# Kernel tuning notes

Hardware: AMD Instinct MI355X
Metric: run time of the kernel (lower is better)

Reference implementation:

```python
import jax, jax.numpy as jnp
import numpy as np

D = 1024
H = 16
HD = D // H
B = 4
L = 2048
FFN = 4 * D
EPS = 1e-5


def _layer_norm(x, g, b):
    mu = jnp.mean(x, axis=-1, keepdims=True)
    var = jnp.mean(jnp.square(x - mu), axis=-1, keepdims=True)
    return (x - mu) * jax.lax.rsqrt(var + EPS) * g + b


def setup_inputs() -> dict:
    key = jax.random.key(0)
    ks = jax.random.split(key, 16)
    s = 1.0 / np.sqrt(D)
    inp = {
        "x": jax.random.normal(ks[0], (B, L, D), dtype=jnp.float32),
        "rel_pos_bias": jax.random.normal(ks[1], (1, H, L, L), dtype=jnp.float32) * 0.02,
        "wq": jax.random.normal(ks[2], (D, D), dtype=jnp.float32) * s,
        "bq": jnp.zeros((D,), jnp.float32),
        "wk": jax.random.normal(ks[3], (D, D), dtype=jnp.float32) * s,
        "bk": jnp.zeros((D,), jnp.float32),
        "wv": jax.random.normal(ks[4], (D, D), dtype=jnp.float32) * s,
        "bv": jnp.zeros((D,), jnp.float32),
        "wo": jax.random.normal(ks[5], (D, D), dtype=jnp.float32) * s,
        "bo": jnp.zeros((D,), jnp.float32),
        "g1": jnp.ones((D,), jnp.float32),
        "be1": jnp.zeros((D,), jnp.float32),
        "g2": jnp.ones((D,), jnp.float32),
        "be2": jnp.zeros((D,), jnp.float32),
        "w1": jax.random.normal(ks[6], (D, FFN), dtype=jnp.float32) * s,
        "bf1": jnp.zeros((FFN,), jnp.float32),
        "w2": jax.random.normal(ks[7], (FFN, D), dtype=jnp.float32) * (1.0 / np.sqrt(FFN)),
        "bf2": jnp.zeros((D,), jnp.float32),
    }
    return inp


def reference(x, rel_pos_bias, wq, bq, wk, bk, wv, bv, wo, bo,
              g1, be1, g2, be2, w1, bf1, w2, bf2):
    scale = HD ** -0.5
    residual = x
    xn = _layer_norm(x, g1, be1)
    # projections -> (B, H, L, HD)
    q = (xn @ wq + bq).reshape(B, L, H, HD).transpose(0, 2, 1, 3)
    k = (xn @ wk + bk).reshape(B, L, H, HD).transpose(0, 2, 1, 3)
    v = (xn @ wv + bv).reshape(B, L, H, HD).transpose(0, 2, 1, 3)
    scores = jnp.einsum('bhqd,bhkd->bhqk', q, k) * scale
    causal = jnp.tril(jnp.ones((L, L), dtype=bool))
    scores = jnp.where(causal[None, None], scores, -jnp.inf)
    scores = scores + rel_pos_bias
    attn = jax.nn.softmax(scores, axis=-1)
    out = jnp.einsum('bhqk,bhkd->bhqd', attn, v)
    out = out.transpose(0, 2, 1, 3).reshape(B, L, D)
    out = out @ wo + bo
    x = residual + out
    residual = x
    xn = _layer_norm(x, g2, be2)
    h = jax.nn.relu(xn @ w1 + bf1)
    x = residual + (h @ w2 + bf2)
    return x
```

## Files before the change

### kernel.cpp

```cpp
#include <hip/hip_runtime.h>
#include <hip/hip_bf16.h>

#define D_   1024
#define H_   16
#define HD_  64
#define B_   4
#define L_   2048
#define FFN_ 4096
#define M_   (B_ * L_)

typedef __bf16 bf16x8 __attribute__((ext_vector_type(8)));
typedef float f32x4 __attribute__((ext_vector_type(4)));
typedef unsigned short ushort8 __attribute__((ext_vector_type(8)));
typedef unsigned short ushort4v __attribute__((ext_vector_type(4)));

__device__ inline unsigned short f2bf(float f) {
    unsigned int u = __float_as_uint(f);
    u += 0x7fff + ((u >> 16) & 1);
    return (unsigned short)(u >> 16);
}
__device__ inline float bf2f(unsigned short u) {
    return __uint_as_float(((unsigned int)u) << 16);
}

__device__ inline void gl_lds16(const unsigned short* g, unsigned short* l) {
    __builtin_amdgcn_global_load_lds(
        (const __attribute__((address_space(1))) unsigned int*)g,
        (__attribute__((address_space(3))) unsigned int*)l, 16, 0, 0);
}

__global__ __launch_bounds__(256) void k_transpose_bf16(
    const float* __restrict__ in, unsigned short* __restrict__ out, int K, int N)
{
    __shared__ float tile[64][65];
    int k0 = blockIdx.y * 64, n0 = blockIdx.x * 64;
    int t = threadIdx.x;
    int r = t >> 2, cs = (t & 3) * 16;
    const float* src = in + (size_t)(k0 + r) * N + n0 + cs;
#pragma unroll
    for (int i = 0; i < 16; i += 4) {
        float4 v = *(const float4*)(src + i);
        tile[r][cs + i + 0] = v.x;
        tile[r][cs + i + 1] = v.y;
        tile[r][cs + i + 2] = v.z;
        tile[r][cs + i + 3] = v.w;
    }
    __syncthreads();
    unsigned short* dst = out + (size_t)(n0 + r) * K + k0 + cs;
#pragma unroll
    for (int i = 0; i < 16; ++i) dst[i] = f2bf(tile[cs + i][r]);
}

__global__ void k_concat_bias(const float* __restrict__ bq, const float* __restrict__ bk,
                              const float* __restrict__ bv, float* __restrict__ out)
{
    int i = blockIdx.x * 256 + threadIdx.x;
    float v = (i < 1024) ? bq[i] : (i < 2048 ? bk[i - 1024] : bv[i - 2048]);
    out[i] = v;
}

__global__ __launch_bounds__(256) void k_layernorm(
    const float* __restrict__ x, const float* __restrict__ g, const float* __restrict__ be,
    unsigned short* __restrict__ out)
{
    int row = blockIdx.x;
    const float* xr = x + (size_t)row * D_;
    int t = threadIdx.x;
    float4 v = *(const float4*)(xr + t * 4);
    float s = v.x + v.y + v.z + v.w;
    float sq = v.x * v.x + v.y * v.y + v.z * v.z + v.w * v.w;
#pragma unroll
    for (int off = 32; off >= 1; off >>= 1) {
        s  += __shfl_down(s, off);
        sq += __shfl_down(sq, off);
    }
    __shared__ float ps[4], psq[4];
    int w = t >> 6;
    if ((t & 63) == 0) { ps[w] = s; psq[w] = sq; }
    __syncthreads();
    float tot  = ps[0] + ps[1] + ps[2] + ps[3];
    float totq = psq[0] + psq[1] + psq[2] + psq[3];
    float mu  = tot * (1.f / D_);
    float var = totq * (1.f / D_) - mu * mu;
    float inv = rsqrtf(var + 1e-5f);
    float4 gv = *(const float4*)(g + t * 4);
    float4 bv = *(const float4*)(be + t * 4);
    ushort4v o;
    o[0] = f2bf((v.x - mu) * inv * gv.x + bv.x);
    o[1] = f2bf((v.y - mu) * inv * gv.y + bv.y);
    o[2] = f2bf((v.z - mu) * inv * gv.z + bv.z);
    o[3] = f2bf((v.w - mu) * inv * gv.w + bv.w);
    *(ushort4v*)(out + (size_t)row * D_ + t * 4) = o;
}

template <int BN, int WGN, bool OUT_BF16, bool RELU, bool RESID>
__global__ __launch_bounds__(512, 2) void k_gemm2(
    const unsigned short* __restrict__ A, const unsigned short* __restrict__ Bt,
    const float* __restrict__ bias, const float* __restrict__ resid,
    void* __restrict__ Cout, int M, int N, int K)
{
    constexpr int WGM = 8 / WGN;
    constexpr int MS = 256 / WGM;
    constexpr int NS = BN / WGN;
    constexpr int MI = MS / 16;
    constexpr int NI = NS / 16;

    __shared__ unsigned short sA[2][256 * 32];
    __shared__ unsigned short sB[2][BN * 32];

    int nwg = gridDim.x, flat = blockIdx.x;
    int wg = (flat & 7) * (nwg >> 3) + (flat >> 3);
    int gx = N / BN;
    int m0 = (wg / gx) * 256, n0 = (wg % gx) * BN;

    int tid = threadIdx.x, lane = tid & 63, wv = tid >> 6;
    int wr = wv / WGN, wc = wv % WGN;
    int wm = wr * MS, wn = wc * NS;
    int lr = lane & 15, qd = lane >> 4;

    f32x4 acc[MI][NI] = {};

    int srow = lane >> 2, scol = (lane & 3) * 8;
    const unsigned short* gA0 = A + (size_t)(m0 + wv * 16 + srow) * K + scol;
    const unsigned short* gA1 = gA0 + (size_t)128 * K;
    const unsigned short* gB0 = Bt + (size_t)(n0 + wv * 16 + srow) * K + scol;
    const unsigned short* gB1 = gB0 + (size_t)128 * K;
    int lb0 = (wv * 16) * 32, lb1 = (wv * 16 + 128) * 32;

    gl_lds16(gA0, &sA[0][lb0]);
    gl_lds16(gA1, &sA[0][lb1]);
    gl_lds16(gB0, &sB[0][lb0]);
    if constexpr (BN == 256) gl_lds16(gB1, &sB[0][lb1]);

    int nk = K >> 5;
    for (int ki = 0; ki < nk; ++ki) {
        int cur = ki & 1;
        __syncthreads();
        if (ki + 1 < nk) {
            int k1 = (ki + 1) << 5;
            gl_lds16(gA0 + k1, &sA[cur ^ 1][lb0]);
            gl_lds16(gA1 + k1, &sA[cur ^ 1][lb1]);
            gl_lds16(gB0 + k1, &sB[cur ^ 1][lb0]);
            if constexpr (BN == 256) gl_lds16(gB1 + k1, &sB[cur ^ 1][lb1]);
        }
        bf16x8 af[MI], bfr[NI];
#pragma unroll
        for (int i = 0; i < MI; ++i)
            af[i] = *(const bf16x8*)(&sA[cur][(wm + i * 16 + lr) * 32 + qd * 8]);
#pragma unroll
        for (int i = 0; i < NI; ++i)
            bfr[i] = *(const bf16x8*)(&sB[cur][(wn + i * 16 + lr) * 32 + qd * 8]);
        __builtin_amdgcn_s_setprio(1);
#pragma unroll
        for (int mi = 0; mi < MI; ++mi)
#pragma unroll
            for (int ni = 0; ni < NI; ++ni)
                acc[mi][ni] = __builtin_amdgcn_mfma_f32_16x16x32_bf16(
                    af[mi], bfr[ni], acc[mi][ni], 0, 0, 0);
        __builtin_amdgcn_s_setprio(0);
    }

#pragma unroll
    for (int ni = 0; ni < NI; ++ni) {
        int col = n0 + wn + ni * 16 + lr;
        float bvv = bias[col];
#pragma unroll
        for (int mi = 0; mi < MI; ++mi) {
#pragma unroll
            for (int r = 0; r < 4; ++r) {
                int row = m0 + wm + mi * 16 + qd * 4 + r;
                float v = acc[mi][ni][r] + bvv;
                if (RELU) v = fmaxf(v, 0.f);
                if (RESID) v += resid[(size_t)row * N + col];
                if (OUT_BF16)
                    ((unsigned short*)Cout)[(size_t)row * N + col] = f2bf(v);
                else
                    ((float*)Cout)[(size_t)row * N + col] = v;
            }
        }
    }
}

__global__ __launch_bounds__(256, 4) void k_attn(
    const unsigned short* __restrict__ qkv, const float* __restrict__ rpb,
    unsigned short* __restrict__ out)
{
    __shared__ unsigned short Ks[64 * 72];
    __shared__ unsigned short Vt[64 * 64];
    __shared__ unsigned short Sp[64 * 72];

    int flat = blockIdx.x;
    int xcd = flat & 7, b = (flat >> 3) & 3, hi = flat >> 5;
    int g = hi * 8 + xcd;
    int h = g & 15;
    int qt = 31 - (g >> 4);
    int q0 = qt * 64;

    int t = threadIdx.x, lane = t & 63, w = t >> 6;
    int lr = lane & 15, qd = lane >> 4;
    int sr = t >> 2, ss = (t & 3) * 16;
    int bL = b * L_;

    bf16x8 aq[2];
    {
        const unsigned short* qsrc =
            qkv + (size_t)(bL + q0 + w * 16 + lr) * 3072 + h * 64 + qd * 8;
        aq[0] = *(const bf16x8*)qsrc;
        aq[1] = *(const bf16x8*)(qsrc + 32);
    }

    f32x4 oacc[4] = {};
    float m_r[4], l_r[4];
#pragma unroll
    for (int r = 0; r < 4; ++r) { m_r[r] = -1e30f; l_r[r] = 0.f; }

    int qrow_base = q0 + w * 16 + qd * 4;
    int ntile = qt + 1;

    ushort8 krA, krB, vrA, vrB;
    {
        const unsigned short* kb_ = qkv + (size_t)(bL + sr) * 3072 + 1024 + h * 64 + ss;
        krA = *(const ushort8*)kb_;  krB = *(const ushort8*)(kb_ + 8);
        vrA = *(const ushort8*)(kb_ + 1024); vrB = *(const ushort8*)(kb_ + 1032);
    }

    for (int kt = 0; kt < ntile; ++kt) {
        int k0 = kt * 64;
        if (kt) __syncthreads();

        *(ushort8*)(Ks + sr * 72 + ss)     = krA;
        *(ushort8*)(Ks + sr * 72 + ss + 8) = krB;

        {
            int role = sr & 1;
            int srp  = sr & ~1;
#pragma unroll
            for (int i = 0; i < 8; ++i) {
                int sendv = role ? (int)(unsigned int)vrA[i] : (int)(unsigned int)vrB[i];
                int got = __shfl_xor(sendv, 4);
                int d = role ? (ss + 8 + i) : (ss + i);
                unsigned short lo = role ? (unsigned short)got : vrA[i];
                unsigned short hi = role ? vrB[i] : (unsigned short)got;
                int swz = (d ^ (d >> 3)) & 7;
                unsigned int u = (unsigned int)lo | ((unsigned int)hi << 16);
                *(unsigned int*)(Vt + d * 64 + (srp ^ (swz << 3))) = u;
            }
        }
        __syncthreads();

        float rv[4][4];
        {
            const float* rpb_base = rpb + ((size_t)h * L_ + qrow_base) * L_ + k0;
#pragma unroll
            for (int r = 0; r < 4; ++r)
#pragma unroll
                for (int nt = 0; nt < 4; ++nt)
                    rv[r][nt] = rpb_base[(size_t)r * L_ + nt * 16 + lr];
        }

        if (kt + 1 < ntile) {
            const unsigned short* kb_ =
                qkv + (size_t)(bL + k0 + 64 + sr) * 3072 + 1024 + h * 64 + ss;
            krA = *(const ushort8*)kb_;  krB = *(const ushort8*)(kb_ + 8);
            vrA = *(const ushort8*)(kb_ + 1024); vrB = *(const ushort8*)(kb_ + 1032);
        }

        f32x4 sc4[4] = {};
        __builtin_amdgcn_s_setprio(1);
#pragma unroll
        for (int ks = 0; ks < 2; ++ks) {
#pragma unroll
            for (int nt = 0; nt < 4; ++nt) {
                bf16x8 bk8 = *(const bf16x8*)(Ks + (nt * 16 + lr) * 72 + ks * 32 + qd * 8);
                sc4[nt] = __builtin_amdgcn_mfma_f32_16x16x32_bf16(aq[ks], bk8, sc4[nt], 0, 0, 0);
            }
        }
        __builtin_amdgcn_s_setprio(0);

        bool last = (kt == qt);
        float pvv[4][4], mx[4];
#pragma unroll
        for (int r = 0; r < 4; ++r) {
            mx[r] = -1e30f;
#pragma unroll
            for (int nt = 0; nt < 4; ++nt) {
                float sv = sc4[nt][r] * 0.125f + rv[r][nt];
                if (last && (k0 + nt * 16 + lr > qrow_base + r)) sv = -1e30f;
                pvv[r][nt] = sv;
                mx[r] = fmaxf(mx[r], sv);
            }
        }
#pragma unroll
        for (int r = 0; r < 4; ++r) {
            mx[r] = fmaxf(mx[r], __shfl_xor(mx[r], 1));
            mx[r] = fmaxf(mx[r], __shfl_xor(mx[r], 2));
            mx[r] = fmaxf(mx[r], __shfl_xor(mx[r], 4));
            mx[r] = fmaxf(mx[r], __shfl_xor(mx[r], 8));
        }
#pragma unroll
        for (int r = 0; r < 4; ++r) {
            float mnew  = fmaxf(m_r[r], mx[r]);
            float alpha = __expf(m_r[r] - mnew);
            float psum = 0.f;
#pragma unroll
            for (int nt = 0; nt < 4; ++nt) {
                float p = __expf(pvv[r][nt] - mnew);
                psum += p;
                Sp[(w * 16 + qd * 4 + r) * 72 + nt * 16 + lr] = f2bf(p);
            }
            psum += __shfl_xor(psum, 1);
            psum += __shfl_xor(psum, 2);
            psum += __shfl_xor(psum, 4);
            psum += __shfl_xor(psum, 8);
            l_r[r] = l_r[r] * alpha + psum;
            m_r[r] = mnew;
            oacc[0][r] *= alpha; oacc[1][r] *= alpha;
            oacc[2][r] *= alpha; oacc[3][r] *= alpha;
        }

        __builtin_amdgcn_s_setprio(1);
#pragma unroll
        for (int ks = 0; ks < 2; ++ks) {
            bf16x8 ap = *(const bf16x8*)(Sp + (w * 16 + lr) * 72 + ks * 32 + qd * 8);
#pragma unroll
            for (int dt = 0; dt < 4; ++dt) {
                int d = dt * 16 + lr;
                int swz = (d ^ (d >> 3)) & 7;
                bf16x8 bv8 = *(const bf16x8*)(Vt + d * 64 + ((ks * 32 + qd * 8) ^ (swz << 3)));
                oacc[dt] = __builtin_amdgcn_mfma_f32_16x16x32_bf16(ap, bv8, oacc[dt], 0, 0, 0);
            }
        }
        __builtin_amdgcn_s_setprio(0);
    }

#pragma unroll
    for (int r = 0; r < 4; ++r) {
        float linv = 1.f / l_r[r];
        int qrow = q0 + w * 16 + qd * 4 + r;
        unsigned short* dst = out + (size_t)(bL + qrow) * 1024 + h * 64;
#pragma unroll
        for (int dt = 0; dt < 4; ++dt)
            dst[dt * 16 + lr] = f2bf(oacc[dt][r] * linv);
    }
}

extern "C" void kernel_launch(void* const* d_in, const int* in_sizes, int n_in,
                              void* d_out, int out_size, void* d_ws, size_t ws_size,
                              hipStream_t stream)
{
    const float* x   = (const float*)d_in[0];
    const float* rpb = (const float*)d_in[1];
    const float* wq  = (const float*)d_in[2];
    const float* bq  = (const float*)d_in[3];
    const float* wk  = (const float*)d_in[4];
    const float* bk  = (const float*)d_in[5];
    const float* wv  = (const float*)d_in[6];
    const float* bv  = (const float*)d_in[7];
    const float* wo  = (const float*)d_in[8];
    const float* bo  = (const float*)d_in[9];
    const float* g1  = (const float*)d_in[10];
    const float* be1 = (const float*)d_in[11];
    const float* g2  = (const float*)d_in[12];
    const float* be2 = (const float*)d_in[13];
    const float* w1  = (const float*)d_in[14];
    const float* bf1 = (const float*)d_in[15];
    const float* w2  = (const float*)d_in[16];
    const float* bf2 = (const float*)d_in[17];
    float* out = (float*)d_out;
    char* ws = (char*)d_ws;

    unsigned short* xn1   = (unsigned short*)(ws + 0);
    unsigned short* qkv   = (unsigned short*)(ws + 16777216);
    unsigned short* attno = (unsigned short*)(ws + 0);
    unsigned short* hbuf  = (unsigned short*)(ws + 0);
    float*          xmid  = (float*)(ws + 67108864);
    unsigned short* xn2   = (unsigned short*)(ws + 100663296);
    unsigned short* wqkvT = (unsigned short*)(ws + 117440512);
    unsigned short* woT   = (unsigned short*)(ws + 123731968);
    unsigned short* w1T   = (unsigned short*)(ws + 125829120);
    unsigned short* w2T   = (unsigned short*)(ws + 134217728);
    float*          bqkv  = (float*)(ws + 142606336);

    k_transpose_bf16<<<dim3(16, 16), 256, 0, stream>>>(wq, wqkvT,                1024, 1024);
    k_transpose_bf16<<<dim3(16, 16), 256, 0, stream>>>(wk, wqkvT + 1024 * 1024,  1024, 1024);
    k_transpose_bf16<<<dim3(16, 16), 256, 0, stream>>>(wv, wqkvT + 2048 * 1024,  1024, 1024);
    k_transpose_bf16<<<dim3(16, 16), 256, 0, stream>>>(wo, woT,                  1024, 1024);
    k_transpose_bf16<<<dim3(64, 16), 256, 0, stream>>>(w1, w1T,                  1024, 4096);
    k_transpose_bf16<<<dim3(16, 64), 256, 0, stream>>>(w2, w2T,                  4096, 1024);
    k_concat_bias<<<12, 256, 0, stream>>>(bq, bk, bv, bqkv);

    k_layernorm<<<M_, 256, 0, stream>>>(x, g1, be1, xn1);
    k_gemm2<128, 2, true, false, false><<<dim3(768), 512, 0, stream>>>(
        xn1, wqkvT, bqkv, nullptr, qkv, M_, 3072, 1024);
    k_attn<<<dim3(2048), 256, 0, stream>>>(qkv, rpb, attno);
    k_gemm2<128, 2, false, false, true><<<dim3(256), 512, 0, stream>>>(
        attno, woT, bo, x, xmid, M_, 1024, 1024);
    k_layernorm<<<M_, 256, 0, stream>>>(xmid, g2, be2, xn2);
    k_gemm2<256, 4, true, true, false><<<dim3(512), 512, 0, stream>>>(
        xn2, w1T, bf1, nullptr, hbuf, M_, 4096, 1024);
    k_gemm2<128, 2, false, false, true><<<dim3(256), 512, 0, stream>>>(
        hbuf, w2T, bf2, xmid, out, M_, 1024, 4096);
}
```

Baseline: 896.1 us.

## Rewrite GEMM with K=64 stages, XOR-swizzled LDS, and templated tile shapes

Replaces the GEMM kernel with a generalized template that stages 64-wide K slices instead of 32, writes LDS with an XOR swizzle to avoid bank conflicts on fragment reads, and parameterizes block and wave tile shapes. The QKV GEMM moves to 256x256 tiles, and the N=1024 GEMMs move to 128x128 tiles with 256 threads and more blocks. Halving the number of K iterations cuts barrier overhead, and the swizzle targets LDS read conflicts. The cost is doubled LDS per buffer and different occupancy per shape.

```diff
diff --git a/kernel.cpp b/kernel.cpp
--- a/kernel.cpp
+++ b/kernel.cpp
@@ -18,9 +18,6 @@
     unsigned int u = __float_as_uint(f);
     u += 0x7fff + ((u >> 16) & 1);
     return (unsigned short)(u >> 16);
-}
-__device__ inline float bf2f(unsigned short u) {
-    return __uint_as_float(((unsigned int)u) << 16);
 }
 
 __device__ inline void gl_lds16(const unsigned short* g, unsigned short* l) {
@@ -93,71 +90,93 @@
     *(ushort4v*)(out + (size_t)row * D_ + t * 4) = o;
 }
 
-template <int BN, int WGN, bool OUT_BF16, bool RELU, bool RESID>
-__global__ __launch_bounds__(512, 2) void k_gemm2(
+template <int BM, int BN, int WM, int WN, bool OUT_BF16, bool RELU, bool RESID>
+__global__ __launch_bounds__(WM * WN * 64, 2) void k_gemm3(
     const unsigned short* __restrict__ A, const unsigned short* __restrict__ Bt,
     const float* __restrict__ bias, const float* __restrict__ resid,
     void* __restrict__ Cout, int M, int N, int K)
 {
-    constexpr int WGM = 8 / WGN;
-    constexpr int MS = 256 / WGM;
-    constexpr int NS = BN / WGN;
-    constexpr int MI = MS / 16;
-    constexpr int NI = NS / 16;
-
-    __shared__ unsigned short sA[2][256 * 32];
-    __shared__ unsigned short sB[2][BN * 32];
+    constexpr int NW  = WM * WN;
+    constexpr int MS  = BM / WM;
+    constexpr int NS  = BN / WN;
+    constexpr int MI  = MS / 16;
+    constexpr int NI  = NS / 16;
+    constexpr int APW = BM / (8 * NW);
+    constexpr int BPW = BN / (8 * NW);
+
+    __shared__ unsigned short sA[2][BM * 64];
+    __shared__ unsigned short sB[2][BN * 64];
 
     int nwg = gridDim.x, flat = blockIdx.x;
     int wg = (flat & 7) * (nwg >> 3) + (flat >> 3);
     int gx = N / BN;
-    int m0 = (wg / gx) * 256, n0 = (wg % gx) * BN;
+    int m0 = (wg / gx) * BM, n0 = (wg % gx) * BN;
 
     int tid = threadIdx.x, lane = tid & 63, wv = tid >> 6;
-    int wr = wv / WGN, wc = wv % WGN;
+    int wr = wv / WN, wc = wv % WN;
     int wm = wr * MS, wn = wc * NS;
     int lr = lane & 15, qd = lane >> 4;
 
     f32x4 acc[MI][NI] = {};
 
-    int srow = lane >> 2, scol = (lane & 3) * 8;
-    const unsigned short* gA0 = A + (size_t)(m0 + wv * 16 + srow) * K + scol;
-    const unsigned short* gA1 = gA0 + (size_t)128 * K;
-    const unsigned short* gB0 = Bt + (size_t)(n0 + wv * 16 + srow) * K + scol;
-    const unsigned short* gB1 = gB0 + (size_t)128 * K;
-    int lb0 = (wv * 16) * 32, lb1 = (wv * 16 + 128) * 32;
-
-    gl_lds16(gA0, &sA[0][lb0]);
-    gl_lds16(gA1, &sA[0][lb1]);
-    gl_lds16(gB0, &sB[0][lb0]);
-    if constexpr (BN == 256) gl_lds16(gB1, &sB[0][lb1]);
-
-    int nk = K >> 5;
+    int r8 = lane >> 3, c8 = lane & 7;
+    int csw = ((c8 ^ (r8 & 7)) * 8);
+    const unsigned short* gA[APW];
+    const unsigned short* gB[BPW];
+    int laA[APW], laB[BPW];
+#pragma unroll
+    for (int s = 0; s < APW; ++s) {
+        int rl = wv * 8 * APW + s * 8;
+        gA[s]  = A + (size_t)(m0 + rl + r8) * K + csw;
+        laA[s] = rl * 64;
+    }
+#pragma unroll
+    for (int s = 0; s < BPW; ++s) {
+        int rl = wv * 8 * BPW + s * 8;
+        gB[s]  = Bt + (size_t)(n0 + rl + r8) * K + csw;
+        laB[s] = rl * 64;
+    }
+
+#pragma unroll
+    for (int s = 0; s < APW; ++s) gl_lds16(gA[s], &sA[0][laA[s]]);
+#pragma unroll
+    for (int s = 0; s < BPW; ++s) gl_lds16(gB[s], &sB[0][laB[s]]);
+
+    int nk = K >> 6;
     for (int ki = 0; ki < nk; ++ki) {
         int cur = ki & 1;
         __syncthreads();
         if (ki + 1 < nk) {
-            int k1 = (ki + 1) << 5;
-            gl_lds16(gA0 + k1, &sA[cur ^ 1][lb0]);
-            gl_lds16(gA1 + k1, &sA[cur ^ 1][lb1]);
-            gl_lds16(gB0 + k1, &sB[cur ^ 1][lb0]);
-            if constexpr (BN == 256) gl_lds16(gB1 + k1, &sB[cur ^ 1][lb1]);
-        }
-        bf16x8 af[MI], bfr[NI];
-#pragma unroll
-        for (int i = 0; i < MI; ++i)
-            af[i] = *(const bf16x8*)(&sA[cur][(wm + i * 16 + lr) * 32 + qd * 8]);
-#pragma unroll
-        for (int i = 0; i < NI; ++i)
-            bfr[i] = *(const bf16x8*)(&sB[cur][(wn + i * 16 + lr) * 32 + qd * 8]);
-        __builtin_amdgcn_s_setprio(1);
-#pragma unroll
-        for (int mi = 0; mi < MI; ++mi)
-#pragma unroll
-            for (int ni = 0; ni < NI; ++ni)
-                acc[mi][ni] = __builtin_amdgcn_mfma_f32_16x16x32_bf16(
-                    af[mi], bfr[ni], acc[mi][ni], 0, 0, 0);
-        __builtin_amdgcn_s_setprio(0);
+            int k1 = (ki + 1) << 6;
+#pragma unroll
+            for (int s = 0; s < APW; ++s) gl_lds16(gA[s] + k1, &sA[cur ^ 1][laA[s]]);
+#pragma unroll
+            for (int s = 0; s < BPW; ++s) gl_lds16(gB[s] + k1, &sB[cur ^ 1][laB[s]]);
+        }
+#pragma unroll
+        for (int ks = 0; ks < 2; ++ks) {
+            bf16x8 af[MI], bfr[NI];
+#pragma unroll
+            for (int i = 0; i < MI; ++i) {
+                int row = wm + i * 16 + lr;
+                int p = ((ks * 4 + qd) ^ (lr & 7)) * 8;
+                af[i] = *(const bf16x8*)(&sA[cur][row * 64 + p]);
+            }
+#pragma unroll
+            for (int i = 0; i < NI; ++i) {
+                int row = wn + i * 16 + lr;
+                int p = ((ks * 4 + qd) ^ (lr & 7)) * 8;
+                bfr[i] = *(const bf16x8*)(&sB[cur][row * 64 + p]);
+            }
+            __builtin_amdgcn_s_setprio(1);
+#pragma unroll
+            for (int mi = 0; mi < MI; ++mi)
+#pragma unroll
+                for (int ni = 0; ni < NI; ++ni)
+                    acc[mi][ni] = __builtin_amdgcn_mfma_f32_16x16x32_bf16(
+                        af[mi], bfr[ni], acc[mi][ni], 0, 0, 0);
+            __builtin_amdgcn_s_setprio(0);
+        }
     }
 
 #pragma unroll
@@ -390,14 +409,14 @@
     k_concat_bias<<<12, 256, 0, stream>>>(bq, bk, bv, bqkv);
 
     k_layernorm<<<M_, 256, 0, stream>>>(x, g1, be1, xn1);
-    k_gemm2<128, 2, true, false, false><<<dim3(768), 512, 0, stream>>>(
+    k_gemm3<256, 256, 2, 4, true, false, false><<<dim3(384), 512, 0, stream>>>(
         xn1, wqkvT, bqkv, nullptr, qkv, M_, 3072, 1024);
     k_attn<<<dim3(2048), 256, 0, stream>>>(qkv, rpb, attno);
-    k_gemm2<128, 2, false, false, true><<<dim3(256), 512, 0, stream>>>(
+    k_gemm3<128, 128, 2, 2, false, false, true><<<dim3(512), 256, 0, stream>>>(
         attno, woT, bo, x, xmid, M_, 1024, 1024);
     k_layernorm<<<M_, 256, 0, stream>>>(xmid, g2, be2, xn2);
-    k_gemm2<256, 4, true, true, false><<<dim3(512), 512, 0, stream>>>(
+    k_gemm3<256, 256, 2, 4, true, true, false><<<dim3(512), 512, 0, stream>>>(
         xn2, w1T, bf1, nullptr, hbuf, M_, 4096, 1024);
-    k_gemm2<128, 2, false, false, true><<<dim3(256), 512, 0, stream>>>(
+    k_gemm3<128, 128, 2, 2, false, false, true><<<dim3(512), 256, 0, stream>>>(
         hbuf, w2T, bf2, xmid, out, M_, 1024, 4096);
 }
```

Result: faster. 846.4 us (-5.5%).
